# Optimization experiments

Measured on AMD Instinct MI355X. Metric: run time of the kernel, lower is better.

Reference implementation:

```python
import math
import jax, jax.numpy as jnp
import numpy as np

HEADS, HD = 16, 64  # head_dim = hidden_size // num_heads = 1024 // 16

def _c(a):
    # a: [2, ...] stacked (real, imag) -> complex64
    return jax.lax.complex(a[0], a[1])

def setup_inputs() -> dict:
    key = jax.random.key(0)
    ks = jax.random.split(key, 16)
    B, S, L, H = 2, 2048, 2048, 1024  # batch, chunk len, cache len, hidden
    w_scale = 1.0 / math.sqrt(2 * H)  # complex fan-in scaling
    d = {
        "hidden":  jax.random.normal(ks[0], (2, B, S, H), jnp.float32),
        "k_cache": jax.random.normal(ks[1], (2, B, L, HEADS, HD), jnp.float32),
        "v_cache": jax.random.normal(ks[2], (2, B, L, HEADS, HD), jnp.float32),
        "qw": jax.random.normal(ks[3], (2, H, H), jnp.float32) * w_scale,
        "qb": jax.random.normal(ks[4], (2, H), jnp.float32) * 0.01,
        "kw": jax.random.normal(ks[5], (2, H, H), jnp.float32) * w_scale,
        "kb": jax.random.normal(ks[6], (2, H), jnp.float32) * 0.01,
        "vw": jax.random.normal(ks[7], (2, H, H), jnp.float32) * w_scale,
        "vb": jax.random.normal(ks[8], (2, H), jnp.float32) * 0.01,
        "ow": jax.random.normal(ks[9], (2, H, H), jnp.float32) * w_scale,
        "ob": jax.random.normal(ks[10], (2, H), jnp.float32) * 0.01,
        "ln_gamma": jnp.stack([jnp.ones(H, jnp.float32) + 0.01 * jax.random.normal(ks[11], (H,)),
                               0.01 * jax.random.normal(ks[12], (H,))]),
        "ln_beta":  0.01 * jax.random.normal(ks[13], (2, H), jnp.float32),
    }
    return d

def _complex_layernorm(x, gamma, beta, eps=1e-5):
    mu = jnp.mean(x, axis=-1, keepdims=True)              # complex mean
    xc = x - mu
    var = jnp.mean(xc.real**2 + xc.imag**2, axis=-1, keepdims=True)
    return xc / jnp.sqrt(var + eps) * gamma + beta

def _clin(z, w, b):
    # complex linear: z [..., in] @ W^T [out, in] + b [out]
    return jnp.einsum('bsh,oh->bso', z, _c(w)) + _c(b)

def reference(hidden, k_cache, v_cache, qw, qb, kw, kb, vw, vb, ow, ob, ln_gamma, ln_beta):
    x = _c(hidden)                                        # [B,S,H] complex64
    B, S, H = x.shape
    normed = _complex_layernorm(x, _c(ln_gamma), _c(ln_beta))
    Q = _clin(normed, qw, qb).reshape(B, S, HEADS, HD)
    K_new = _clin(normed, kw, kb).reshape(B, S, HEADS, HD)
    V_new = _clin(normed, vw, vb).reshape(B, S, HEADS, HD)
    K = jnp.concatenate([_c(k_cache), K_new], axis=1)     # [B, L+S, nh, hd]
    V = jnp.concatenate([_c(v_cache), V_new], axis=1)
    cache_len = k_cache.shape[2]
    kv = K.shape[1]                                       # == window_size here
    # Hermitian score: Re(Q K^dagger) / sqrt(hd)
    scores = jnp.einsum('bqhd,bkhd->bhqk', Q, jnp.conj(K)).real / math.sqrt(HD)
    row = jnp.arange(S)[:, None]
    col = jnp.arange(kv)[None, :]
    # prefix (cache) fully visible; causal within the new chunk
    mask = jnp.where((col >= cache_len) & (col - cache_len > row), -jnp.inf, 0.0).astype(scores.dtype)
    w = jax.nn.softmax(scores + mask[None, None], axis=-1)  # real weights
    out = jax.lax.complex(jnp.einsum('bhqk,bkhd->bqhd', w, V.real),
                          jnp.einsum('bhqk,bkhd->bqhd', w, V.imag)).reshape(B, S, H)
    delta = _clin(out, ow, ob)
    y = x + delta
    out_stacked = jnp.stack([y.real, y.imag])             # [2,B,S,H]
    new_k = jnp.stack([K.real, K.imag])                   # [2,B,window,nh,hd]
    new_v = jnp.stack([V.real, V.imag])
    return (out_stacked, new_k, new_v)
```

## Files before the change

kernel.cpp:

```cpp
#include <hip/hip_runtime.h>

#define HEADS 16
#define SEQ   2048
#define HID   1024
#define CACHE 2048
#define KVLEN 4096
#define MROWS 4096
#define KD    2048

typedef float  f32x4  __attribute__((ext_vector_type(4)));
typedef __bf16 bf16x4 __attribute__((ext_vector_type(4)));
typedef __bf16 bf16x8 __attribute__((ext_vector_type(8)));

__device__ __forceinline__ void gload_lds16(const void* g, void* l) {
  __builtin_amdgcn_global_load_lds((const __attribute__((address_space(1))) void*)g,
                                   (__attribute__((address_space(3))) void*)l, 16, 0, 0);
}

__global__ __launch_bounds__(256) void k_layernorm(const float* __restrict__ hid,
                                                   const float* __restrict__ gamma,
                                                   const float* __restrict__ beta,
                                                   __bf16* __restrict__ normed) {
  int row = blockIdx.x;
  int t = threadIdx.x;
  const float* xr = hid + (size_t)row * HID;
  const float* xi = hid + (size_t)MROWS * HID + (size_t)row * HID;
  float vr[4], vi[4];
  float sr = 0.f, si = 0.f;
#pragma unroll
  for (int i = 0; i < 4; i++) { int h = t + i * 256; vr[i] = xr[h]; vi[i] = xi[h]; sr += vr[i]; si += vi[i]; }
  __shared__ float red[2][4];
  for (int m = 1; m < 64; m <<= 1) { sr += __shfl_xor(sr, m); si += __shfl_xor(si, m); }
  int wid = t >> 6, l = t & 63;
  if (l == 0) { red[0][wid] = sr; red[1][wid] = si; }
  __syncthreads();
  float mr = (red[0][0] + red[0][1] + red[0][2] + red[0][3]) * (1.0f / HID);
  float mi = (red[1][0] + red[1][1] + red[1][2] + red[1][3]) * (1.0f / HID);
  float sv = 0.f;
#pragma unroll
  for (int i = 0; i < 4; i++) { float a = vr[i] - mr, b = vi[i] - mi; sv += a * a + b * b; }
  for (int m = 1; m < 64; m <<= 1) sv += __shfl_xor(sv, m);
  __syncthreads();
  if (l == 0) red[0][wid] = sv;
  __syncthreads();
  float var = (red[0][0] + red[0][1] + red[0][2] + red[0][3]) * (1.0f / HID);
  float inv = rsqrtf(var + 1e-5f);
  __bf16* outr = normed + (size_t)row * KD;
#pragma unroll
  for (int i = 0; i < 4; i++) {
    int h = t + i * 256;
    float a = (vr[i] - mr) * inv, b = (vi[i] - mi) * inv;
    float gr = gamma[h], gi = gamma[HID + h], br = beta[h], bi = beta[HID + h];
    outr[h]       = (__bf16)(a * gr - b * gi + br);
    outr[HID + h] = (__bf16)(a * gi + b * gr + bi);
  }
}

__global__ __launch_bounds__(256) void k_packw(const float* __restrict__ qw, const float* __restrict__ kw,
                                               const float* __restrict__ vw, const float* __restrict__ ow,
                                               __bf16* __restrict__ dst) {
  int idx = blockIdx.x * 256 + threadIdx.x;
  int sel = idx >> 19;
  int li  = idx & 524287;
  const float* w = sel == 0 ? qw : (sel == 1 ? kw : (sel == 2 ? vw : ow));
  int o  = li >> 8;
  int k0 = (li & 255) * 8;
  const float* wr = w;
  const float* wi = w + HID * HID;
  int oimag = (o >= HID);
  int oo = o & (HID - 1);
  bf16x8 v;
#pragma unroll
  for (int j = 0; j < 8; j++) {
    int k = k0 + j;
    int kim = (k >= HID);
    int kk = k & (HID - 1);
    float x;
    if (!oimag) x = kim ? -wi[oo * HID + kk] : wr[oo * HID + kk];
    else        x = kim ?  wr[oo * HID + kk] : wi[oo * HID + kk];
    v[j] = (__bf16)x;
  }
  *(bf16x8*)(dst + ((size_t)sel << 22) + (size_t)o * KD + k0) = v;
}

__global__ __launch_bounds__(256) void k_copyk(const float* __restrict__ kc,
                                               float* __restrict__ nk,
                                               __bf16* __restrict__ Ka) {
  int li = blockIdx.x * 256 + threadIdx.x;
  int c4 = li & 255;
  int kv = (li >> 8) & 2047;
  int b  = (li >> 19) & 1;
  int p  = (li >> 20) & 1;
  f32x4 v = *(const f32x4*)(kc + (((size_t)((p * 2 + b) * 2048 + kv)) << 10) + c4 * 4);
  *(f32x4*)(nk + ((((size_t)(p * 2 + b)) * KVLEN + kv) << 10) + c4 * 4) = v;
  int h = c4 >> 4, d = (c4 & 15) * 4;
  bf16x4 w;
#pragma unroll
  for (int j = 0; j < 4; j++) w[j] = (__bf16)v[j];
  *(bf16x4*)(Ka + (((size_t)(b * 16 + h)) * KVLEN + kv) * 128 + p * 64 + d) = w;
}

__global__ __launch_bounds__(256) void k_buildv(const float* __restrict__ vc,
                                                float* __restrict__ nv,
                                                __bf16* __restrict__ dst) {
  __shared__ float tile[32][129];
  int kt = blockIdx.x;
  int bh = blockIdx.y;
  int b = bh >> 4, h = bh & 15;
  int t = threadIdx.x;
  int kv0 = kt * 32;
#pragma unroll
  for (int i = 0; i < 16; i++) {
    int idx = i * 256 + t;
    int kvl = idx >> 7, dsl = idx & 127;
    int p = dsl >> 6, d = dsl & 63;
    float v = vc[(((size_t)(p * 2 + b)) * CACHE + kv0 + kvl) * HID + h * 64 + d];
    tile[kvl][dsl] = v;
    nv[(((size_t)(p * 2 + b)) * KVLEN + kv0 + kvl) * HID + h * 64 + d] = v;
  }
  __syncthreads();
#pragma unroll
  for (int i = 0; i < 16; i++) {
    int idx = i * 256 + t;
    int dsl = idx >> 5, kvl = idx & 31;
    dst[(((size_t)bh) * 128 + dsl) * KVLEN + kv0 + kvl] = (__bf16)tile[kvl][dsl];
  }
}

#define BM 128
#define BN 128
#define BK 64
template <int QKV>
__global__ __launch_bounds__(256, 3) void k_gemm(const __bf16* __restrict__ A,
                                                 const __bf16* __restrict__ Bp,
                                                 const float* __restrict__ bias0,
                                                 const float* __restrict__ bias1,
                                                 const float* __restrict__ bias2,
                                                 const float* __restrict__ hid,
                                                 float* __restrict__ outF0,
                                                 float* __restrict__ outF1,
                                                 __bf16* __restrict__ outB0,
                                                 __bf16* __restrict__ outB1,
                                                 __bf16* __restrict__ outB2) {
  __shared__ __align__(16) __bf16 As[BM * BK];
  __shared__ __align__(16) __bf16 Bs[BN * BK];
  int bm0 = blockIdx.x * BM, bn0 = blockIdx.y * BN;
  int t = threadIdx.x, l = t & 63, wid = t >> 6;
  int wr = wid >> 1, wc = wid & 1;
  int l15 = l & 15, lg = l >> 4;
  f32x4 acc[4][4];
  f32x4 zero = {0.f, 0.f, 0.f, 0.f};
#pragma unroll
  for (int i = 0; i < 4; i++)
#pragma unroll
    for (int j = 0; j < 4; j++) acc[i][j] = zero;
  const __bf16* Ab = A + (size_t)bm0 * KD;
  const __bf16* Bb = Bp + (size_t)bn0 * KD;
  for (int k0 = 0; k0 < KD; k0 += BK) {
#pragma unroll
    for (int c = 0; c < 4; c++) {
      int idx = c * 256 + t;
      int row = idx >> 3, ch = idx & 7;
      int chs = ch ^ (row & 7);
      gload_lds16(Ab + (size_t)row * KD + k0 + chs * 8, As + idx * 8);
      gload_lds16(Bb + (size_t)row * KD + k0 + chs * 8, Bs + idx * 8);
    }
    __syncthreads();
#pragma unroll
    for (int ks = 0; ks < 2; ks++) {
      bf16x8 af[4], bfv[4];
#pragma unroll
      for (int i = 0; i < 4; i++) {
        int ra = wr * 64 + i * 16 + l15;
        int rb = wc * 64 + i * 16 + l15;
        af[i]  = *(const bf16x8*)((const char*)As + ra * 128 + ((ks * 64 + lg * 16) ^ ((ra & 7) << 4)));
        bfv[i] = *(const bf16x8*)((const char*)Bs + rb * 128 + ((ks * 64 + lg * 16) ^ ((rb & 7) << 4)));
      }
#pragma unroll
      for (int mi = 0; mi < 4; mi++)
#pragma unroll
        for (int ni = 0; ni < 4; ni++)
          acc[mi][ni] = __builtin_amdgcn_mfma_f32_16x16x32_bf16(af[mi], bfv[ni], acc[mi][ni], 0, 0, 0);
    }
    __syncthreads();
  }
#pragma unroll
  for (int mi = 0; mi < 4; mi++) {
#pragma unroll
    for (int ni = 0; ni < 4; ni++) {
      int mbase = bm0 + wr * 64 + mi * 16 + lg * 4;
      int n = bn0 + wc * 64 + ni * 16 + l15;
      int b = mbase >> 11, sbase = mbase & 2047;
      if (QKV) {
        int mode = n >> 11, nl = n & 2047;
        const float* bias = mode == 0 ? bias0 : (mode == 1 ? bias1 : bias2);
        float bv = bias[nl];
        int p = nl >> 10, hd = nl & 1023;
        if (mode == 2) {
          bf16x4 w;
#pragma unroll
          for (int j = 0; j < 4; j++) {
            float v = acc[mi][ni][j] + bv;
            outF1[(((size_t)(p * 2 + b)) * KVLEN + (CACHE + sbase + j)) * HID + hd] = v;
            w[j] = (__bf16)v;
          }
          *(bf16x4*)(outB2 + (((size_t)(b * 16 + (hd >> 6))) * 128 + p * 64 + (hd & 63)) * KVLEN + CACHE + sbase) = w;
        } else {
#pragma unroll
          for (int j = 0; j < 4; j++) {
            float v = acc[mi][ni][j] + bv;
            int s = sbase + j;
            if (mode == 0) {
              outB0[(((size_t)(b * 16 + (hd >> 6))) * SEQ + s) * 128 + p * 64 + (hd & 63)] = (__bf16)v;
            } else {
              outF0[(((size_t)(p * 2 + b)) * KVLEN + (CACHE + s)) * HID + hd] = v;
              outB1[(((size_t)(b * 16 + (hd >> 6))) * KVLEN + (CACHE + s)) * 128 + p * 64 + (hd & 63)] = (__bf16)v;
            }
          }
        }
      } else {
        float bv = bias0[n];
        int p = n >> 10;
#pragma unroll
        for (int j = 0; j < 4; j++) {
          float v = acc[mi][ni][j] + bv;
          size_t off = (((size_t)(p * 2 + b)) * SEQ + (sbase + j)) * HID + (n & 1023);
          outF0[off] = v + hid[off];
        }
      }
    }
  }
}

__global__ __launch_bounds__(512, 4) void k_attn(const __bf16* __restrict__ Q,
                                                 const __bf16* __restrict__ Kt,
                                                 const __bf16* __restrict__ Vt,
                                                 __bf16* __restrict__ outp) {
  __shared__ __align__(16) __bf16 Ks[2][64 * 128];
  __shared__ __align__(16) __bf16 Vs[2][128 * 64];
  __shared__ __align__(16) __bf16 Ps[8][16 * 64];
  int id = blockIdx.y * gridDim.x + blockIdx.x;
  int xcd = id & 7, li = id >> 3;
  int bh = (xcd << 2) | (li >> 4);
  int ql = li & 15;
  int qt = (ql & 1) ? (15 - (ql >> 1)) : (ql >> 1);
  int b = bh >> 4, h = bh & 15;
  int t = threadIdx.x, l = t & 63, wid = t >> 6;
  int l15 = l & 15, lg = l >> 4;
  const __bf16* Qb = Q + ((size_t)bh * SEQ) * 128;
  const __bf16* Kb = Kt + ((size_t)bh * KVLEN) * 128;
  const __bf16* Vb = Vt + ((size_t)bh * 128) * KVLEN;
  __bf16* Pw = &Ps[wid][0];
  int q0 = qt * 128 + wid * 16;
  bf16x8 aQ[4];
#pragma unroll
  for (int dk = 0; dk < 4; dk++)
    aQ[dk] = *(const bf16x8*)(Qb + (size_t)(q0 + l15) * 128 + dk * 32 + lg * 8);
  f32x4 zero = {0.f, 0.f, 0.f, 0.f};
  f32x4 o[8];
  f32x4 sums = zero;
#pragma unroll
  for (int df = 0; df < 8; df++) o[df] = zero;
  bf16x8 ones;
#pragma unroll
  for (int i = 0; i < 8; i++) ones[i] = (__bf16)1.0f;
  const int nfull = 32 + 2 * qt;
  const int nt = nfull + 2;
  int sw = (l15 & 7) << 4;
  int rx = (l15 & 7) << 3;

  auto STAGE = [&](int bb, int ti) {
    int kv0 = ti * 64;
#pragma unroll
    for (int c = 0; c < 2; c++) {
      int idx = c * 512 + t;
      int kr = idx >> 4;
      gload_lds16(Kb + (size_t)(kv0 + kr) * 128 + (((idx & 15) ^ (kr & 7)) << 3), &Ks[bb][idx * 8]);
      int vr = idx >> 3;
      gload_lds16(Vb + (size_t)vr * KVLEN + kv0 + (((idx & 7) ^ (vr & 7)) << 3), &Vs[bb][idx * 8]);
    }
  };

  STAGE(0, 0);
  for (int ti = 0; ti < nt; ti++) {
    int bb = ti & 1;
    if (ti + 1 < nt) {
      STAGE(bb ^ 1, ti + 1);
      asm volatile("s_waitcnt vmcnt(4)" ::: "memory");
    } else {
      asm volatile("s_waitcnt vmcnt(0)" ::: "memory");
    }
    __builtin_amdgcn_s_barrier();
    const char* KsB = (const char*)&Ks[bb][0];
    const char* VsB = (const char*)&Vs[bb][0];
    f32x4 sacc[4];
    __builtin_amdgcn_s_setprio(1);
#pragma unroll
    for (int kvf = 0; kvf < 4; kvf++) {
      sacc[kvf] = zero;
      const char* kbase = KsB + (kvf * 16 + l15) * 256;
#pragma unroll
      for (int dk = 0; dk < 4; dk++) {
        bf16x8 bK = *(const bf16x8*)(kbase + ((dk * 64 + lg * 16) ^ sw));
        sacc[kvf] = __builtin_amdgcn_mfma_f32_16x16x32_bf16(bK, aQ[dk], sacc[kvf], 0, 0, 0);
      }
    }
    __builtin_amdgcn_s_setprio(0);
    bool masked = (ti >= nfull);
    int lim = qt * 128 + wid * 16 + l15 - (ti - 32) * 64;
#pragma unroll
    for (int kvf = 0; kvf < 4; kvf++) {
      bf16x4 w;
#pragma unroll
      for (int j = 0; j < 4; j++) {
        float p = exp2f(sacc[kvf][j] * 0.18033688011112042f);
        if (masked && (kvf * 16 + lg * 4 + j > lim)) p = 0.f;
        w[j] = (__bf16)p;
      }
      *(bf16x4*)(Pw + l15 * 64 + ((kvf * 16 + lg * 4) ^ rx)) = w;
    }
    __builtin_amdgcn_s_setprio(1);
#pragma unroll
    for (int ks = 0; ks < 2; ks++) {
      bf16x8 aP = *(const bf16x8*)(Pw + l15 * 64 + ((ks * 32 + lg * 8) ^ rx));
      sums = __builtin_amdgcn_mfma_f32_16x16x32_bf16(aP, ones, sums, 0, 0, 0);
      int off = (ks * 64 + lg * 16) ^ sw;
#pragma unroll
      for (int df = 0; df < 8; df++) {
        bf16x8 bV = *(const bf16x8*)(VsB + (df * 16 + l15) * 128 + off);
        o[df] = __builtin_amdgcn_mfma_f32_16x16x32_bf16(aP, bV, o[df], 0, 0, 0);
      }
    }
    __builtin_amdgcn_s_setprio(0);
    __builtin_amdgcn_s_barrier();
  }
  float inv[4];
#pragma unroll
  for (int j = 0; j < 4; j++) inv[j] = 1.0f / sums[j];
#pragma unroll
  for (int df = 0; df < 8; df++) {
    int dslot = df * 16 + l15;
    int col = (dslot < 64) ? (h * 64 + dslot) : (1024 + h * 64 + (dslot - 64));
#pragma unroll
    for (int j = 0; j < 4; j++) {
      int qg2 = q0 + lg * 4 + j;
      float v = o[df][j] * inv[j];
      outp[((size_t)(b * SEQ + qg2)) * KD + col] = (__bf16)v;
    }
  }
}

extern "C" void kernel_launch(void* const* d_in, const int* in_sizes, int n_in,
                              void* d_out, int out_size, void* d_ws, size_t ws_size,
                              hipStream_t stream) {
  const float* hid = (const float*)d_in[0];
  const float* kc  = (const float*)d_in[1];
  const float* vc  = (const float*)d_in[2];
  const float* qw  = (const float*)d_in[3];
  const float* qb  = (const float*)d_in[4];
  const float* kw  = (const float*)d_in[5];
  const float* kb  = (const float*)d_in[6];
  const float* vw  = (const float*)d_in[7];
  const float* vb  = (const float*)d_in[8];
  const float* ow  = (const float*)d_in[9];
  const float* ob  = (const float*)d_in[10];
  const float* lg  = (const float*)d_in[11];
  const float* lb  = (const float*)d_in[12];

  float* y  = (float*)d_out;
  float* nk = y + 8388608;
  float* nv = nk + 16777216;

  char* ws = (char*)d_ws;
  __bf16* normed = (__bf16*)(ws);
  __bf16* wall   = (__bf16*)(ws + 16777216);
  __bf16* Qa     = (__bf16*)(ws + 50331648);
  __bf16* Ka     = (__bf16*)(ws + 67108864);
  __bf16* Va     = (__bf16*)(ws + 100663296);
  __bf16* ao     = (__bf16*)(ws + 134217728);

  k_layernorm<<<4096, 256, 0, stream>>>(hid, lg, lb, normed);
  k_packw<<<8192, 256, 0, stream>>>(qw, kw, vw, ow, wall);
  k_copyk<<<8192, 256, 0, stream>>>(kc, nk, Ka);
  dim3 gv(64, 32);
  k_buildv<<<gv, 256, 0, stream>>>(vc, nv, Va);
  dim3 gq(32, 48);
  k_gemm<1><<<gq, 256, 0, stream>>>(normed, wall, qb, kb, vb, nullptr, nk, nv, Qa, Ka, Va);
  dim3 ga(16, 32);
  k_attn<<<ga, 512, 0, stream>>>(Qa, Ka, Va, ao);
  dim3 go(32, 16);
  k_gemm<0><<<go, 256, 0, stream>>>(ao, wall + ((size_t)3 << 22), ob, nullptr, nullptr, hid, y, nullptr, nullptr, nullptr, nullptr);
}
```

Baseline: 434.9 us.

## Use 256x256 double-buffered tiled GEMM with XCD-aware block mapping for QKV projection

Replaces the 128x128 single-buffered QKV GEMM with a dedicated 256x256-tile kernel using 512 threads, double-buffered LDS staged via direct global-to-LDS loads interleaved with MFMA work, and a block-id remap that groups N tiles per XCD for L2 reuse. It also raises MFMA priority around the compute sections. The aim is to cut global traffic per FLOP and hide load latency behind compute. The cost is heavier LDS use (128KB), which lowers occupancy, and a 384-block grid that may leave some CUs underused. The output GEMM is split into its own non-template kernel.

```diff
diff --git a/kernel.cpp b/kernel.cpp
--- a/kernel.cpp
+++ b/kernel.cpp
@@ -127,21 +127,143 @@
   }
 }
 
+__global__ __launch_bounds__(512, 2) void k_gemm256(const __bf16* __restrict__ A,
+                                                    const __bf16* __restrict__ Bp,
+                                                    const float* __restrict__ qb,
+                                                    const float* __restrict__ kb,
+                                                    const float* __restrict__ vb,
+                                                    float* __restrict__ nk,
+                                                    float* __restrict__ nv,
+                                                    __bf16* __restrict__ Qa,
+                                                    __bf16* __restrict__ Ka,
+                                                    __bf16* __restrict__ Va) {
+  __shared__ __align__(16) __bf16 As[2][256 * 64];
+  __shared__ __align__(16) __bf16 Bs[2][256 * 64];
+  int id = blockIdx.y * gridDim.x + blockIdx.x;
+  int xcd = id & 7, li = id >> 3;
+  int nb = xcd * 3 + (li >> 4);
+  int mb = li & 15;
+  int bm0 = mb * 256, bn0 = nb * 256;
+  int mode = nb >> 3;
+  int t = threadIdx.x, l = t & 63, wid = t >> 6;
+  int wm = wid >> 2, wn = wid & 3;
+  int l15 = l & 15, lg = l >> 4;
+  int sw = (l15 & 7) << 4;
+  f32x4 acc[8][4];
+  f32x4 zero = {0.f, 0.f, 0.f, 0.f};
+#pragma unroll
+  for (int i = 0; i < 8; i++)
+#pragma unroll
+    for (int j = 0; j < 4; j++) acc[i][j] = zero;
+  const __bf16* Ab = A + (size_t)bm0 * KD;
+  const __bf16* Bb = Bp + (size_t)bn0 * KD;
+
+  auto STAGEH = [&](const __bf16* src, __bf16* dst, int k0) {
+#pragma unroll
+    for (int c = 0; c < 2; c++) {
+      int idx = c * 512 + t;
+      int row = idx >> 3, slot = idx & 7;
+      gload_lds16(src + (size_t)row * KD + k0 + ((slot ^ (row & 7)) << 3),
+                  dst + row * 64 + slot * 8);
+    }
+  };
+
+  STAGEH(Ab, &As[0][0], 0);
+  STAGEH(Ab + (size_t)128 * KD, &As[0][8192], 0);
+  STAGEH(Bb, &Bs[0][0], 0);
+  STAGEH(Bb + (size_t)128 * KD, &Bs[0][8192], 0);
+  asm volatile("s_waitcnt vmcnt(0)" ::: "memory");
+  __builtin_amdgcn_s_barrier();
+
+  const int NT = KD / 64;
+  for (int tt = 0; tt < NT; tt++) {
+    int bb = tt & 1;
+    const char* AsB = (const char*)&As[bb][0];
+    const char* BsB = (const char*)&Bs[bb][0];
+    int k1 = (tt + 1) * 64;
+    bf16x8 bF[4][2];
+#pragma unroll
+    for (int nf = 0; nf < 4; nf++) {
+      int rb = wn * 64 + nf * 16 + l15;
+#pragma unroll
+      for (int kk = 0; kk < 2; kk++)
+        bF[nf][kk] = *(const bf16x8*)(BsB + rb * 128 + ((kk * 64 + lg * 16) ^ sw));
+    }
+#pragma unroll
+    for (int p = 0; p < 4; p++) {
+      if (tt + 1 < NT) {
+        if (p == 0)      STAGEH(Ab, &As[bb ^ 1][0], k1);
+        else if (p == 1) STAGEH(Ab + (size_t)128 * KD, &As[bb ^ 1][8192], k1);
+        else if (p == 2) STAGEH(Bb, &Bs[bb ^ 1][0], k1);
+        else             STAGEH(Bb + (size_t)128 * KD, &Bs[bb ^ 1][8192], k1);
+      }
+      bf16x8 aF[2][2];
+#pragma unroll
+      for (int i = 0; i < 2; i++) {
+        int ra = wm * 128 + (p * 2 + i) * 16 + l15;
+#pragma unroll
+        for (int kk = 0; kk < 2; kk++)
+          aF[i][kk] = *(const bf16x8*)(AsB + ra * 128 + ((kk * 64 + lg * 16) ^ sw));
+      }
+      __builtin_amdgcn_s_setprio(1);
+#pragma unroll
+      for (int i = 0; i < 2; i++)
+#pragma unroll
+        for (int nf = 0; nf < 4; nf++)
+#pragma unroll
+          for (int kk = 0; kk < 2; kk++)
+            acc[p * 2 + i][nf] =
+                __builtin_amdgcn_mfma_f32_16x16x32_bf16(aF[i][kk], bF[nf][kk], acc[p * 2 + i][nf], 0, 0, 0);
+      __builtin_amdgcn_s_setprio(0);
+    }
+    asm volatile("s_waitcnt vmcnt(0)" ::: "memory");
+    __builtin_amdgcn_s_barrier();
+  }
+  const float* bias = mode == 0 ? qb : (mode == 1 ? kb : vb);
+#pragma unroll
+  for (int mf = 0; mf < 8; mf++) {
+#pragma unroll
+    for (int nf = 0; nf < 4; nf++) {
+      int mbase = bm0 + wm * 128 + mf * 16 + lg * 4;
+      int n = bn0 + wn * 64 + nf * 16 + l15;
+      int b = mbase >> 11, sbase = mbase & 2047;
+      int nl = n & 2047;
+      float bv = bias[nl];
+      int p = nl >> 10, hd = nl & 1023;
+      if (mode == 2) {
+        bf16x4 w;
+#pragma unroll
+        for (int j = 0; j < 4; j++) {
+          float v = acc[mf][nf][j] + bv;
+          nv[(((size_t)(p * 2 + b)) * KVLEN + (CACHE + sbase + j)) * HID + hd] = v;
+          w[j] = (__bf16)v;
+        }
+        *(bf16x4*)(Va + (((size_t)(b * 16 + (hd >> 6))) * 128 + p * 64 + (hd & 63)) * KVLEN + CACHE + sbase) = w;
+      } else {
+#pragma unroll
+        for (int j = 0; j < 4; j++) {
+          float v = acc[mf][nf][j] + bv;
+          int s = sbase + j;
+          if (mode == 0) {
+            Qa[(((size_t)(b * 16 + (hd >> 6))) * SEQ + s) * 128 + p * 64 + (hd & 63)] = (__bf16)v;
+          } else {
+            nk[(((size_t)(p * 2 + b)) * KVLEN + (CACHE + s)) * HID + hd] = v;
+            Ka[(((size_t)(b * 16 + (hd >> 6))) * KVLEN + (CACHE + s)) * 128 + p * 64 + (hd & 63)] = (__bf16)v;
+          }
+        }
+      }
+    }
+  }
+}
+
 #define BM 128
 #define BN 128
 #define BK 64
-template <int QKV>
-__global__ __launch_bounds__(256, 3) void k_gemm(const __bf16* __restrict__ A,
-                                                 const __bf16* __restrict__ Bp,
-                                                 const float* __restrict__ bias0,
-                                                 const float* __restrict__ bias1,
-                                                 const float* __restrict__ bias2,
-                                                 const float* __restrict__ hid,
-                                                 float* __restrict__ outF0,
-                                                 float* __restrict__ outF1,
-                                                 __bf16* __restrict__ outB0,
-                                                 __bf16* __restrict__ outB1,
-                                                 __bf16* __restrict__ outB2) {
+__global__ __launch_bounds__(256, 3) void k_gemmO(const __bf16* __restrict__ A,
+                                                  const __bf16* __restrict__ Bp,
+                                                  const float* __restrict__ bias0,
+                                                  const float* __restrict__ hid,
+                                                  float* __restrict__ outF0) {
   __shared__ __align__(16) __bf16 As[BM * BK];
   __shared__ __align__(16) __bf16 Bs[BN * BK];
   int bm0 = blockIdx.x * BM, bn0 = blockIdx.y * BN;
@@ -191,42 +313,13 @@
       int mbase = bm0 + wr * 64 + mi * 16 + lg * 4;
       int n = bn0 + wc * 64 + ni * 16 + l15;
       int b = mbase >> 11, sbase = mbase & 2047;
-      if (QKV) {
-        int mode = n >> 11, nl = n & 2047;
-        const float* bias = mode == 0 ? bias0 : (mode == 1 ? bias1 : bias2);
-        float bv = bias[nl];
-        int p = nl >> 10, hd = nl & 1023;
-        if (mode == 2) {
-          bf16x4 w;
-#pragma unroll
-          for (int j = 0; j < 4; j++) {
-            float v = acc[mi][ni][j] + bv;
-            outF1[(((size_t)(p * 2 + b)) * KVLEN + (CACHE + sbase + j)) * HID + hd] = v;
-            w[j] = (__bf16)v;
-          }
-          *(bf16x4*)(outB2 + (((size_t)(b * 16 + (hd >> 6))) * 128 + p * 64 + (hd & 63)) * KVLEN + CACHE + sbase) = w;
-        } else {
-#pragma unroll
-          for (int j = 0; j < 4; j++) {
-            float v = acc[mi][ni][j] + bv;
-            int s = sbase + j;
-            if (mode == 0) {
-              outB0[(((size_t)(b * 16 + (hd >> 6))) * SEQ + s) * 128 + p * 64 + (hd & 63)] = (__bf16)v;
-            } else {
-              outF0[(((size_t)(p * 2 + b)) * KVLEN + (CACHE + s)) * HID + hd] = v;
-              outB1[(((size_t)(b * 16 + (hd >> 6))) * KVLEN + (CACHE + s)) * 128 + p * 64 + (hd & 63)] = (__bf16)v;
-            }
-          }
-        }
-      } else {
-        float bv = bias0[n];
-        int p = n >> 10;
-#pragma unroll
-        for (int j = 0; j < 4; j++) {
-          float v = acc[mi][ni][j] + bv;
-          size_t off = (((size_t)(p * 2 + b)) * SEQ + (sbase + j)) * HID + (n & 1023);
-          outF0[off] = v + hid[off];
-        }
+      float bv = bias0[n];
+      int p = n >> 10;
+#pragma unroll
+      for (int j = 0; j < 4; j++) {
+        float v = acc[mi][ni][j] + bv;
+        size_t off = (((size_t)(p * 2 + b)) * SEQ + (sbase + j)) * HID + (n & 1023);
+        outF0[off] = v + hid[off];
       }
     }
   }
@@ -384,10 +477,10 @@
   k_copyk<<<8192, 256, 0, stream>>>(kc, nk, Ka);
   dim3 gv(64, 32);
   k_buildv<<<gv, 256, 0, stream>>>(vc, nv, Va);
-  dim3 gq(32, 48);
-  k_gemm<1><<<gq, 256, 0, stream>>>(normed, wall, qb, kb, vb, nullptr, nk, nv, Qa, Ka, Va);
+  dim3 gq(16, 24);
+  k_gemm256<<<gq, 512, 0, stream>>>(normed, wall, qb, kb, vb, nk, nv, Qa, Ka, Va);
   dim3 ga(16, 32);
   k_attn<<<ga, 512, 0, stream>>>(Qa, Ka, Va, ao);
   dim3 go(32, 16);
-  k_gemm<0><<<go, 256, 0, stream>>>(ao, wall + ((size_t)3 << 22), ob, nullptr, nullptr, hid, y, nullptr, nullptr, nullptr, nullptr);
-}
+  k_gemmO<<<go, 256, 0, stream>>>(ao, wall + ((size_t)3 << 22), ob, hid, y);
+}
```

After: 506.7 us. +16.5%, slower.
